# Kernel tuning notes

Measured on AMD Instinct MI355X. Metric: run time of the kernel, lower is better.

Reference implementation:

```python
import jax, jax.numpy as jnp
import numpy as np

BETA = 100.0
H = 2048
W = 2048


def setup_inputs() -> dict:
    key = jax.random.key(0)
    heatmap = jax.random.normal(key, (1, 11, H, W), dtype=jnp.float32)
    return {"heatmap": heatmap}


def _soft_argmax(hm, xx, yy):
    # hm: (..., H, W); softmax over flattened H*W, then coordinate expectation
    flat = hm.reshape(hm.shape[:-2] + (hm.shape[-2] * hm.shape[-1],))
    sm = jax.nn.softmax(flat, axis=-1).reshape(hm.shape)
    ax = jnp.sum(sm * xx, axis=(-2, -1))
    ay = jnp.sum(sm * yy, axis=(-2, -1))
    return ax, ay


def reference(heatmap):
    b, n, h, w = heatmap.shape  # structurally b=1, n=11
    dt = heatmap.dtype
    hm = heatmap * jnp.asarray(BETA, dt)
    yy = jnp.broadcast_to(jnp.arange(h, dtype=dt)[:, None], (h, w))
    xx = jnp.broadcast_to(jnp.arange(w, dtype=dt)[None, :], (h, w))

    # init: channels 9,10 (last two), full-map soft-argmax
    ax, ay = _soft_argmax(hm[0, -2:], xx, yy)  # (2,), (2,)
    out = jnp.zeros((11, 2), dt)
    out = out.at[9:11, 0].set(ax).at[9:11, 1].set(ay)
    dis0 = out[10, 1] - out[9, 1]

    channels = hm[0, :9][::-1]  # iterate i = 8 .. 0
    idxs = jnp.arange(8, -1, -1)
    rows = jnp.arange(h, dtype=dt)[:, None]  # (H,1) row coordinates for band mask

    def body(carry, xs):
        out, dis, dis_sum, dis_num = carry
        i, ch = xs
        y_ip1 = jax.lax.dynamic_slice(out, (i + 1, 1), (1, 1))[0, 0]
        y_ip2 = jax.lax.dynamic_slice(out, (i + 2, 1), (1, 1))[0, 0]
        last_y = jnp.floor(y_ip1)            # emulates .long() (y >= 0)
        tmp_dis = jnp.ceil(y_ip2 - y_ip1)
        cond = jnp.abs(tmp_dis - dis) > 0.35 * dis
        dis_sum = jnp.where(cond, dis_sum + tmp_dis, dis_sum)
        dis_num = jnp.where(cond, dis_num + 1.0, dis_num)
        dis = jnp.where(cond, dis_sum / jnp.maximum(dis_num, 1.0), dis)
        start_raw = last_y - 1.8 * dis
        end_y = jnp.round(start_raw + 0.9 * 2.0 * dis)
        start_y = jnp.round(start_raw)
        mask = ((rows >= start_y) & (rows <= end_y)).astype(dt)  # (H,1)
        ax_i, ay_i = _soft_argmax(ch * mask, xx, yy)
        row = jnp.stack([ax_i, ay_i])[None, :]  # (1,2)
        out = jax.lax.dynamic_update_slice(out, row.astype(dt), (i, jnp.zeros((), idxs.dtype)))
        return (out, dis, dis_sum, dis_num), None

    zero = jnp.zeros((), dt)
    (out, _, _, _), _ = jax.lax.scan(body, (out, dis0, zero, zero), (idxs, channels))
    return out[None]  # (1, 11, 2)
```

## Files before the change

### kernel.cpp

```cpp
#include <hip/hip_runtime.h>
#include <math.h>

#define HH 2048
#define WW 2048
#define NB 256

struct Tup { float m, z, sx, sy; };

__device__ __forceinline__ void comb(Tup& a, const Tup& b) {
  float Mn = fmaxf(a.m, b.m);
  float w1 = (a.m == Mn) ? 1.0f : expf(a.m - Mn);
  float w2 = (b.m == Mn) ? 1.0f : expf(b.m - Mn);
  a.z  = a.z  * w1 + b.z  * w2;
  a.sx = a.sx * w1 + b.sx * w2;
  a.sy = a.sy * w1 + b.sy * w2;
  a.m  = Mn;
}

__device__ Tup row_reduce(const float* __restrict__ rowp) {
  const int tid = threadIdx.x;
  const float4* r4 = (const float4*)rowp;
  float m = -INFINITY, z = 0.0f, sx = 0.0f;
#pragma unroll
  for (int p = 0; p < WW / (4 * NB); ++p) {
    int i4 = tid + NB * p;
    float4 v = r4[i4];
    float vv[4] = {v.x, v.y, v.z, v.w};
    float c0 = (float)(i4 * 4);
#pragma unroll
    for (int k = 0; k < 4; ++k) {
      float x = vv[k] * 100.0f;
      if (x > m) {
        float sc = expf(m - x);
        z  = z  * sc + 1.0f;
        sx = sx * sc + (c0 + (float)k);
        m = x;
      } else {
        float w = expf(x - m);
        z  += w;
        sx += w * (c0 + (float)k);
      }
    }
  }
  __shared__ float sm_[NB], sz_[NB], ss_[NB];
  __syncthreads();
  sm_[tid] = m; sz_[tid] = z; ss_[tid] = sx;
  __syncthreads();
  for (int off = NB / 2; off > 0; off >>= 1) {
    if (tid < off) {
      Tup a = {sm_[tid], sz_[tid], ss_[tid], 0.0f};
      Tup b = {sm_[tid + off], sz_[tid + off], ss_[tid + off], 0.0f};
      comb(a, b);
      sm_[tid] = a.m; sz_[tid] = a.z; ss_[tid] = a.sx;
    }
    __syncthreads();
  }
  Tup t = {sm_[0], sz_[0], ss_[0], 0.0f};
  return t;
}

__device__ Tup block_reduce4(Tup t) {
  __shared__ float am[NB], az[NB], axx[NB], ayy[NB];
  const int tid = threadIdx.x;
  __syncthreads();
  am[tid] = t.m; az[tid] = t.z; axx[tid] = t.sx; ayy[tid] = t.sy;
  __syncthreads();
  for (int off = NB / 2; off > 0; off >>= 1) {
    if (tid < off) {
      Tup a = {am[tid], az[tid], axx[tid], ayy[tid]};
      Tup b = {am[tid + off], az[tid + off], axx[tid + off], ayy[tid + off]};
      comb(a, b);
      am[tid] = a.m; az[tid] = a.z; axx[tid] = a.sx; ayy[tid] = a.sy;
    }
    __syncthreads();
  }
  Tup r = {am[0], az[0], axx[0], ayy[0]};
  return r;
}

__device__ Tup merge_rows(const float4* arr, int s, int e) {
  Tup acc = {-INFINITY, 0.0f, 0.0f, 0.0f};
  for (int r = s + (int)threadIdx.x; r <= e; r += NB) {
    float4 p = arr[r];
    Tup q = {p.x, p.y, p.z, p.y * (float)r};
    comb(acc, q);
  }
  return block_reduce4(acc);
}

__device__ void finalize(Tup acc, int s, int e, bool valid, float& ax, float& ay) {
  float M = acc.m, Z = acc.z, SX = acc.sx, SY = acc.sy;
  int nin = valid ? (e - s + 1) : 0;
  int nout = HH - nin;
  if (nout > 0) {
    float M2 = fmaxf(M, 0.0f);
    float wi = (M == M2) ? 1.0f : expf(M - M2);
    float wo = (M2 == 0.0f) ? 1.0f : expf(-M2);
    Z *= wi; SX *= wi; SY *= wi;
    float nout_e = (float)nout * (float)WW;
    float sox = (float)nout * 2096128.0f;
    float sinr = valid ? (float)(((long)(s + e) * (e - s + 1)) / 2) : 0.0f;
    float soy = (2096128.0f - sinr) * 2048.0f;
    Z  += wo * nout_e;
    SX += wo * sox;
    SY += wo * soy;
  }
  ax = SX / Z; ay = SY / Z;
}


__global__ __launch_bounds__(NB) void k_rows(const float* __restrict__ heat, float* ws) {
  float4* F = (float4*)(ws + 32);
  const int b = blockIdx.x;
  const int ch = 9 + (b >> 11);
  const int r = b & (HH - 1);
  Tup t = row_reduce(heat + ((size_t)ch * HH + r) * WW);
  if (threadIdx.x == 0) F[b] = make_float4(t.m, t.z, t.sx, 0.0f);
}

__global__ __launch_bounds__(NB) void k_step(const float* __restrict__ heat, float* ws,
                                             float* __restrict__ out, int i) {
  float* state = ws;
  float4* F  = (float4*)(ws + 32);
  float4* B0 = F + 4096;
  float4* B1 = B0 + HH;

  float st[28];
  if (i == 8) {
    for (int k = 0; k < 28; ++k) st[k] = 0.0f;
    Tup a9  = merge_rows(F, 0, HH - 1);
    Tup a10 = merge_rows(F + HH, 0, HH - 1);
    float ax, ay;
    finalize(a9,  0, HH - 1, true, ax, ay); st[18] = ax; st[19] = ay;
    finalize(a10, 0, HH - 1, true, ax, ay); st[20] = ax; st[21] = ay;
    st[22] = st[21] - st[19];
    st[23] = 0.0f; st[24] = 0.0f;
  } else {
    for (int k = 0; k < 28; ++k) st[k] = state[k];
    const int j = i + 1;
    const float4* Bprev = (j & 1) ? B1 : B0;
    int s = (int)st[25], e = (int)st[26];
    bool valid = (st[27] != 0.0f);
    Tup acc = {-INFINITY, 0.0f, 0.0f, 0.0f};
    if (valid) acc = merge_rows(Bprev, s, e);
    float ax, ay;
    finalize(acc, s, e, valid, ax, ay);
    st[2 * j] = ax; st[2 * j + 1] = ay;
  }

  if (i >= 0) {
    float y1 = st[2 * (i + 1) + 1];
    float y2 = st[2 * (i + 2) + 1];
    float dis = st[22], dsum = st[23], dnum = st[24];
    float last_y = floorf(y1);
    float tmp = ceilf(y2 - y1);
    bool cond = fabsf(tmp - dis) > 0.35f * dis;
    if (cond) { dsum += tmp; dnum += 1.0f; dis = dsum / fmaxf(dnum, 1.0f); }
    float start_raw = last_y - 1.8f * dis;
    float end_f   = rintf(start_raw + 1.8f * dis);
    float start_f = rintf(start_raw);
    int s2 = (int)fmaxf(start_f, 0.0f);
    int e2 = (int)fminf(end_f, (float)(HH - 1));
    bool bvalid = (s2 <= e2) && (end_f >= 0.0f) && (start_f <= (float)(HH - 1));
    st[22] = dis; st[23] = dsum; st[24] = dnum;
    st[25] = (float)s2; st[26] = (float)e2; st[27] = bvalid ? 1.0f : 0.0f;

    float4* Bcur = (i & 1) ? B1 : B0;
    if (bvalid) {
      for (int r = s2 + (int)blockIdx.x; r <= e2; r += (int)gridDim.x) {
        Tup t = row_reduce(heat + ((size_t)i * HH + r) * WW);
        if (threadIdx.x == 0) Bcur[r] = make_float4(t.m, t.z, t.sx, 0.0f);
      }
    }
    if (blockIdx.x == 0 && threadIdx.x == 0)
      for (int k = 0; k < 28; ++k) state[k] = st[k];
  } else {
    if (blockIdx.x == 0 && threadIdx.x == 0)
      for (int k = 0; k < 22; ++k) out[k] = st[k];
  }
}

extern "C" void kernel_launch(void* const* d_in, const int* in_sizes, int n_in,
                              void* d_out, int out_size, void* d_ws, size_t ws_size,
                              hipStream_t stream) {
  const float* heat = (const float*)d_in[0];
  float* out = (float*)d_out;
  float* ws = (float*)d_ws;
  hipLaunchKernelGGL(k_rows, dim3(2 * HH), dim3(NB), 0, stream, heat, ws);
  for (int i = 8; i >= 0; --i) {
    hipLaunchKernelGGL(k_step, dim3(NB), dim3(NB), 0, stream, heat, ws, out, i);
  }
  hipLaunchKernelGGL(k_step, dim3(1), dim3(NB), 0, stream, heat, ws, out, -1);
}
```

Measured before the change: 244.6 us.

## Precompute per-row softmax stats for all channels, then run the chain in one block

Replaces the per-step band reductions with a single kernel that computes online-softmax row statistics for every row of all 11 channels up front. A single one-block kernel then runs the whole sequential dependency chain, merging only the precomputed row stats in each band. This cuts eleven launches down to two and removes the serial dependency on heatmap reads. In exchange it reads the full heatmap for every channel, including rows outside the bands, and the workspace now needs room for 11*2048 float4 entries.

```diff
diff --git a/kernel.cpp b/kernel.cpp
--- a/kernel.cpp
+++ b/kernel.cpp
@@ -109,49 +109,29 @@
 }
 
 
-__global__ __launch_bounds__(NB) void k_rows(const float* __restrict__ heat, float* ws) {
+__global__ __launch_bounds__(NB) void k_rows_all(const float* __restrict__ heat,
+                                                 float* ws) {
   float4* F = (float4*)(ws + 32);
   const int b = blockIdx.x;
-  const int ch = 9 + (b >> 11);
-  const int r = b & (HH - 1);
-  Tup t = row_reduce(heat + ((size_t)ch * HH + r) * WW);
+  Tup t = row_reduce(heat + (size_t)b * WW);
   if (threadIdx.x == 0) F[b] = make_float4(t.m, t.z, t.sx, 0.0f);
 }
 
-__global__ __launch_bounds__(NB) void k_step(const float* __restrict__ heat, float* ws,
-                                             float* __restrict__ out, int i) {
-  float* state = ws;
-  float4* F  = (float4*)(ws + 32);
-  float4* B0 = F + 4096;
-  float4* B1 = B0 + HH;
+__global__ __launch_bounds__(NB) void k_chain(float* ws, float* __restrict__ out) {
+  const float4* F = (const float4*)(ws + 32);
+  float st[22];
+  float ax, ay;
 
-  float st[28];
-  if (i == 8) {
-    for (int k = 0; k < 28; ++k) st[k] = 0.0f;
-    Tup a9  = merge_rows(F, 0, HH - 1);
-    Tup a10 = merge_rows(F + HH, 0, HH - 1);
-    float ax, ay;
-    finalize(a9,  0, HH - 1, true, ax, ay); st[18] = ax; st[19] = ay;
-    finalize(a10, 0, HH - 1, true, ax, ay); st[20] = ax; st[21] = ay;
-    st[22] = st[21] - st[19];
-    st[23] = 0.0f; st[24] = 0.0f;
-  } else {
-    for (int k = 0; k < 28; ++k) st[k] = state[k];
-    const int j = i + 1;
-    const float4* Bprev = (j & 1) ? B1 : B0;
-    int s = (int)st[25], e = (int)st[26];
-    bool valid = (st[27] != 0.0f);
-    Tup acc = {-INFINITY, 0.0f, 0.0f, 0.0f};
-    if (valid) acc = merge_rows(Bprev, s, e);
-    float ax, ay;
-    finalize(acc, s, e, valid, ax, ay);
-    st[2 * j] = ax; st[2 * j + 1] = ay;
-  }
+  Tup a9 = merge_rows(F + 9 * HH, 0, HH - 1);
+  finalize(a9, 0, HH - 1, true, ax, ay);  st[18] = ax; st[19] = ay;
+  Tup a10 = merge_rows(F + 10 * HH, 0, HH - 1);
+  finalize(a10, 0, HH - 1, true, ax, ay); st[20] = ax; st[21] = ay;
 
-  if (i >= 0) {
+  float dis = st[21] - st[19], dsum = 0.0f, dnum = 0.0f;
+
+  for (int i = 8; i >= 0; --i) {
     float y1 = st[2 * (i + 1) + 1];
     float y2 = st[2 * (i + 2) + 1];
-    float dis = st[22], dsum = st[23], dnum = st[24];
     float last_y = floorf(y1);
     float tmp = ceilf(y2 - y1);
     bool cond = fabsf(tmp - dis) > 0.35f * dis;
@@ -159,25 +139,16 @@
     float start_raw = last_y - 1.8f * dis;
     float end_f   = rintf(start_raw + 1.8f * dis);
     float start_f = rintf(start_raw);
-    int s2 = (int)fmaxf(start_f, 0.0f);
-    int e2 = (int)fminf(end_f, (float)(HH - 1));
-    bool bvalid = (s2 <= e2) && (end_f >= 0.0f) && (start_f <= (float)(HH - 1));
-    st[22] = dis; st[23] = dsum; st[24] = dnum;
-    st[25] = (float)s2; st[26] = (float)e2; st[27] = bvalid ? 1.0f : 0.0f;
+    int s = (int)fmaxf(start_f, 0.0f);
+    int e = (int)fminf(end_f, (float)(HH - 1));
+    bool valid = (s <= e) && (end_f >= 0.0f) && (start_f <= (float)(HH - 1));
+    Tup acc = {-INFINITY, 0.0f, 0.0f, 0.0f};
+    if (valid) acc = merge_rows(F + (size_t)i * HH, s, e);
+    finalize(acc, s, e, valid, ax, ay);
+    st[2 * i] = ax; st[2 * i + 1] = ay;
+  }
 
-    float4* Bcur = (i & 1) ? B1 : B0;
-    if (bvalid) {
-      for (int r = s2 + (int)blockIdx.x; r <= e2; r += (int)gridDim.x) {
-        Tup t = row_reduce(heat + ((size_t)i * HH + r) * WW);
-        if (threadIdx.x == 0) Bcur[r] = make_float4(t.m, t.z, t.sx, 0.0f);
-      }
-    }
-    if (blockIdx.x == 0 && threadIdx.x == 0)
-      for (int k = 0; k < 28; ++k) state[k] = st[k];
-  } else {
-    if (blockIdx.x == 0 && threadIdx.x == 0)
-      for (int k = 0; k < 22; ++k) out[k] = st[k];
-  }
+  if (threadIdx.x < 22) out[threadIdx.x] = st[threadIdx.x];
 }
 
 extern "C" void kernel_launch(void* const* d_in, const int* in_sizes, int n_in,
@@ -186,9 +157,6 @@
   const float* heat = (const float*)d_in[0];
   float* out = (float*)d_out;
   float* ws = (float*)d_ws;
-  hipLaunchKernelGGL(k_rows, dim3(2 * HH), dim3(NB), 0, stream, heat, ws);
-  for (int i = 8; i >= 0; --i) {
-    hipLaunchKernelGGL(k_step, dim3(NB), dim3(NB), 0, stream, heat, ws, out, i);
-  }
-  hipLaunchKernelGGL(k_step, dim3(1), dim3(NB), 0, stream, heat, ws, out, -1);
+  hipLaunchKernelGGL(k_rows_all, dim3(11 * HH), dim3(NB), 0, stream, heat, ws);
+  hipLaunchKernelGGL(k_chain, dim3(1), dim3(NB), 0, stream, ws, out);
 }
```

Measured after the change: 258.7 us. 5.8% more time.

## Reduce rows per wavefront with two-pass max-then-exp and shuffle reductions

Applied to the files above, without the earlier changes.

Each row is now reduced by a single 64-lane wavefront instead of a 256-thread block. Each lane keeps its 32 values in registers, the wave takes the maximum first, and then one exp per element accumulates z and sx. Shared-memory tree reductions with many barriers are replaced by xor-shuffle reductions. The partial merge also becomes a two-pass max-then-sum, the stage grid grows to 512 blocks, and each step writes its state to its own slot. The aim is to cut the branchy online-softmax rescaling and the reduction synchronisation, at the cost of higher register use for the 32-value buffer.

```diff
diff --git a/kernel.cpp b/kernel.cpp
--- a/kernel.cpp
+++ b/kernel.cpp
@@ -4,92 +4,93 @@
 #define HH 2048
 #define WW 2048
 #define NB 256
-
-struct Tup { float m, z, sx, sy; };
-
-__device__ __forceinline__ void comb(Tup& a, const Tup& b) {
-  float Mn = fmaxf(a.m, b.m);
-  float w1 = (a.m == Mn) ? 1.0f : expf(a.m - Mn);
-  float w2 = (b.m == Mn) ? 1.0f : expf(b.m - Mn);
-  a.z  = a.z  * w1 + b.z  * w2;
-  a.sx = a.sx * w1 + b.sx * w2;
-  a.sy = a.sy * w1 + b.sy * w2;
-  a.m  = Mn;
-}
-
-__device__ Tup row_reduce(const float* __restrict__ rowp) {
-  const int tid = threadIdx.x;
+#define STAGE_GRID 512
+
+
+__device__ __forceinline__ float wave_fmax(float v) {
+#pragma unroll
+  for (int m = 1; m < 64; m <<= 1) v = fmaxf(v, __shfl_xor(v, m, 64));
+  return v;
+}
+__device__ __forceinline__ float wave_fsum(float v) {
+#pragma unroll
+  for (int m = 1; m < 64; m <<= 1) v += __shfl_xor(v, m, 64);
+  return v;
+}
+
+__device__ float block_fmax(float v) {
+  __shared__ float s[4];
+  v = wave_fmax(v);
+  __syncthreads();
+  if ((threadIdx.x & 63) == 0) s[threadIdx.x >> 6] = v;
+  __syncthreads();
+  return fmaxf(fmaxf(s[0], s[1]), fmaxf(s[2], s[3]));
+}
+
+__device__ void block_fsum3(float& a, float& b, float& c) {
+  __shared__ float sa[4], sb[4], sc[4];
+  a = wave_fsum(a); b = wave_fsum(b); c = wave_fsum(c);
+  __syncthreads();
+  if ((threadIdx.x & 63) == 0) {
+    int w = threadIdx.x >> 6;
+    sa[w] = a; sb[w] = b; sc[w] = c;
+  }
+  __syncthreads();
+  a = (sa[0] + sa[1]) + (sa[2] + sa[3]);
+  b = (sb[0] + sb[1]) + (sb[2] + sb[3]);
+  c = (sc[0] + sc[1]) + (sc[2] + sc[3]);
+}
+
+__device__ float4 wave_row_partial(const float* __restrict__ rowp) {
+  const int lane = threadIdx.x & 63;
   const float4* r4 = (const float4*)rowp;
-  float m = -INFINITY, z = 0.0f, sx = 0.0f;
-#pragma unroll
-  for (int p = 0; p < WW / (4 * NB); ++p) {
-    int i4 = tid + NB * p;
-    float4 v = r4[i4];
-    float vv[4] = {v.x, v.y, v.z, v.w};
-    float c0 = (float)(i4 * 4);
+  float d[32];
+  float m = -INFINITY;
+#pragma unroll
+  for (int p = 0; p < 8; ++p) {
+    float4 v = r4[lane + 64 * p];
+    d[4 * p + 0] = v.x * 100.0f;
+    d[4 * p + 1] = v.y * 100.0f;
+    d[4 * p + 2] = v.z * 100.0f;
+    d[4 * p + 3] = v.w * 100.0f;
+    m = fmaxf(m, fmaxf(fmaxf(d[4 * p], d[4 * p + 1]), fmaxf(d[4 * p + 2], d[4 * p + 3])));
+  }
+  float M = wave_fmax(m);
+  float z = 0.0f, sx = 0.0f;
+#pragma unroll
+  for (int p = 0; p < 8; ++p) {
+    float c0 = (float)(4 * (lane + 64 * p));
 #pragma unroll
     for (int k = 0; k < 4; ++k) {
-      float x = vv[k] * 100.0f;
-      if (x > m) {
-        float sc = expf(m - x);
-        z  = z  * sc + 1.0f;
-        sx = sx * sc + (c0 + (float)k);
-        m = x;
-      } else {
-        float w = expf(x - m);
-        z  += w;
-        sx += w * (c0 + (float)k);
-      }
+      float e = expf(d[4 * p + k] - M);
+      z += e;
+      sx += e * (c0 + (float)k);
     }
   }
-  __shared__ float sm_[NB], sz_[NB], ss_[NB];
-  __syncthreads();
-  sm_[tid] = m; sz_[tid] = z; ss_[tid] = sx;
-  __syncthreads();
-  for (int off = NB / 2; off > 0; off >>= 1) {
-    if (tid < off) {
-      Tup a = {sm_[tid], sz_[tid], ss_[tid], 0.0f};
-      Tup b = {sm_[tid + off], sz_[tid + off], ss_[tid + off], 0.0f};
-      comb(a, b);
-      sm_[tid] = a.m; sz_[tid] = a.z; ss_[tid] = a.sx;
-    }
-    __syncthreads();
-  }
-  Tup t = {sm_[0], sz_[0], ss_[0], 0.0f};
-  return t;
-}
-
-__device__ Tup block_reduce4(Tup t) {
-  __shared__ float am[NB], az[NB], axx[NB], ayy[NB];
-  const int tid = threadIdx.x;
-  __syncthreads();
-  am[tid] = t.m; az[tid] = t.z; axx[tid] = t.sx; ayy[tid] = t.sy;
-  __syncthreads();
-  for (int off = NB / 2; off > 0; off >>= 1) {
-    if (tid < off) {
-      Tup a = {am[tid], az[tid], axx[tid], ayy[tid]};
-      Tup b = {am[tid + off], az[tid + off], axx[tid + off], ayy[tid + off]};
-      comb(a, b);
-      am[tid] = a.m; az[tid] = a.z; axx[tid] = a.sx; ayy[tid] = a.sy;
-    }
-    __syncthreads();
-  }
-  Tup r = {am[0], az[0], axx[0], ayy[0]};
-  return r;
-}
-
-__device__ Tup merge_rows(const float4* arr, int s, int e) {
-  Tup acc = {-INFINITY, 0.0f, 0.0f, 0.0f};
+  z = wave_fsum(z);
+  sx = wave_fsum(sx);
+  return make_float4(M, z, sx, 0.0f);
+}
+
+__device__ void merge_partials(const float4* __restrict__ arr, int s, int e,
+                               float& M, float& Z, float& SX, float& SY) {
+  float m = -INFINITY;
+  for (int r = s + (int)threadIdx.x; r <= e; r += NB) m = fmaxf(m, arr[r].x);
+  M = block_fmax(m);
+  float z = 0.0f, sx = 0.0f, sy = 0.0f;
   for (int r = s + (int)threadIdx.x; r <= e; r += NB) {
     float4 p = arr[r];
-    Tup q = {p.x, p.y, p.z, p.y * (float)r};
-    comb(acc, q);
-  }
-  return block_reduce4(acc);
-}
-
-__device__ void finalize(Tup acc, int s, int e, bool valid, float& ax, float& ay) {
-  float M = acc.m, Z = acc.z, SX = acc.sx, SY = acc.sy;
+    float w = expf(p.x - M);
+    z  += w * p.y;
+    sx += w * p.z;
+    sy += w * p.y * (float)r;
+  }
+  block_fsum3(z, sx, sy);
+  Z = z; SX = sx; SY = sy;
+}
+
+__device__ void finalize2(float M, float Z, float SX, float SY, int s, int e,
+                          bool valid, float& ax, float& ay) {
   int nin = valid ? (e - s + 1) : 0;
   int nout = HH - nin;
   if (nout > 0) {
@@ -105,46 +106,50 @@
     SX += wo * sox;
     SY += wo * soy;
   }
-  ax = SX / Z; ay = SY / Z;
-}
-
-
-__global__ __launch_bounds__(NB) void k_rows(const float* __restrict__ heat, float* ws) {
-  float4* F = (float4*)(ws + 32);
-  const int b = blockIdx.x;
-  const int ch = 9 + (b >> 11);
-  const int r = b & (HH - 1);
-  Tup t = row_reduce(heat + ((size_t)ch * HH + r) * WW);
-  if (threadIdx.x == 0) F[b] = make_float4(t.m, t.z, t.sx, 0.0f);
-}
-
-__global__ __launch_bounds__(NB) void k_step(const float* __restrict__ heat, float* ws,
-                                             float* __restrict__ out, int i) {
-  float* state = ws;
-  float4* F  = (float4*)(ws + 32);
+  ax = SX / Z;
+  ay = SY / Z;
+}
+
+
+__global__ __launch_bounds__(NB) void k_rows910(const float* __restrict__ heat,
+                                                float* ws) {
+  float4* F = (float4*)(ws + 512);
+  int gw = blockIdx.x * 4 + (threadIdx.x >> 6);
+  int ch = 9 + (gw >> 11);
+  int r = gw & (HH - 1);
+  float4 t = wave_row_partial(heat + ((size_t)ch * HH + r) * WW);
+  if ((threadIdx.x & 63) == 0) F[gw] = t;
+}
+
+__global__ __launch_bounds__(NB) void k_stage(const float* __restrict__ heat,
+                                              float* ws, float* __restrict__ out,
+                                              int i) {
+  float4* F  = (float4*)(ws + 512);
   float4* B0 = F + 4096;
   float4* B1 = B0 + HH;
 
   float st[28];
   if (i == 8) {
     for (int k = 0; k < 28; ++k) st[k] = 0.0f;
-    Tup a9  = merge_rows(F, 0, HH - 1);
-    Tup a10 = merge_rows(F + HH, 0, HH - 1);
-    float ax, ay;
-    finalize(a9,  0, HH - 1, true, ax, ay); st[18] = ax; st[19] = ay;
-    finalize(a10, 0, HH - 1, true, ax, ay); st[20] = ax; st[21] = ay;
+    float M, Z, SX, SY, ax, ay;
+    merge_partials(F, 0, HH - 1, M, Z, SX, SY);
+    finalize2(M, Z, SX, SY, 0, HH - 1, true, ax, ay);
+    st[18] = ax; st[19] = ay;
+    merge_partials(F + HH, 0, HH - 1, M, Z, SX, SY);
+    finalize2(M, Z, SX, SY, 0, HH - 1, true, ax, ay);
+    st[20] = ax; st[21] = ay;
     st[22] = st[21] - st[19];
     st[23] = 0.0f; st[24] = 0.0f;
   } else {
-    for (int k = 0; k < 28; ++k) st[k] = state[k];
+    const float* prev = ws + 32 * (i + 1);
+    for (int k = 0; k < 28; ++k) st[k] = prev[k];
     const int j = i + 1;
     const float4* Bprev = (j & 1) ? B1 : B0;
     int s = (int)st[25], e = (int)st[26];
     bool valid = (st[27] != 0.0f);
-    Tup acc = {-INFINITY, 0.0f, 0.0f, 0.0f};
-    if (valid) acc = merge_rows(Bprev, s, e);
-    float ax, ay;
-    finalize(acc, s, e, valid, ax, ay);
+    float M = -INFINITY, Z = 0.0f, SX = 0.0f, SY = 0.0f, ax, ay;
+    if (valid) merge_partials(Bprev, s, e, M, Z, SX, SY);
+    finalize2(M, Z, SX, SY, s, e, valid, ax, ay);
     st[2 * j] = ax; st[2 * j + 1] = ay;
   }
 
@@ -167,16 +172,18 @@
 
     float4* Bcur = (i & 1) ? B1 : B0;
     if (bvalid) {
-      for (int r = s2 + (int)blockIdx.x; r <= e2; r += (int)gridDim.x) {
-        Tup t = row_reduce(heat + ((size_t)i * HH + r) * WW);
-        if (threadIdx.x == 0) Bcur[r] = make_float4(t.m, t.z, t.sx, 0.0f);
+      const int wid = (int)(blockIdx.x * 4) + (threadIdx.x >> 6);
+      for (int r = s2 + wid; r <= e2; r += (int)gridDim.x * 4) {
+        float4 t = wave_row_partial(heat + ((size_t)i * HH + r) * WW);
+        if ((threadIdx.x & 63) == 0) Bcur[r] = t;
       }
     }
-    if (blockIdx.x == 0 && threadIdx.x == 0)
-      for (int k = 0; k < 28; ++k) state[k] = st[k];
+    if (blockIdx.x == 0 && threadIdx.x == 0) {
+      float* slot = ws + 32 * i;
+      for (int k = 0; k < 28; ++k) slot[k] = st[k];
+    }
   } else {
-    if (blockIdx.x == 0 && threadIdx.x == 0)
-      for (int k = 0; k < 22; ++k) out[k] = st[k];
+    if (blockIdx.x == 0 && threadIdx.x < 22) out[threadIdx.x] = st[threadIdx.x];
   }
 }
 
@@ -186,9 +193,9 @@
   const float* heat = (const float*)d_in[0];
   float* out = (float*)d_out;
   float* ws = (float*)d_ws;
-  hipLaunchKernelGGL(k_rows, dim3(2 * HH), dim3(NB), 0, stream, heat, ws);
+  hipLaunchKernelGGL(k_rows910, dim3(1024), dim3(NB), 0, stream, heat, ws);
   for (int i = 8; i >= 0; --i) {
-    hipLaunchKernelGGL(k_step, dim3(NB), dim3(NB), 0, stream, heat, ws, out, i);
-  }
-  hipLaunchKernelGGL(k_step, dim3(1), dim3(NB), 0, stream, heat, ws, out, -1);
-}
+    hipLaunchKernelGGL(k_stage, dim3(STAGE_GRID), dim3(NB), 0, stream, heat, ws, out, i);
+  }
+  hipLaunchKernelGGL(k_stage, dim3(1), dim3(NB), 0, stream, heat, ws, out, -1);
+}
```

Result: no change. 243.5 us (-0.5%).
